# Kernel optimization log

Hardware: AMD Instinct MI355X
Metric: run time of the kernel (lower is better)

The kernel has to match this reference:

```python
import jax, jax.numpy as jnp
import numpy as np

B, S, D, H, E, K = 4, 2048, 1024, 512, 64, 8


def setup_inputs() -> dict:
    key = jax.random.key(0)
    k1, k2, k3, k4 = jax.random.split(key, 4)
    x = jax.random.normal(k1, (B, S, D), dtype=jnp.float32)
    # gate weight stored as [D, E] (equivalent to torch Linear weight [E, D] transposed)
    Wg = jax.random.normal(k2, (D, E), dtype=jnp.float32) * (1.0 / np.sqrt(D))
    Wup = jax.random.normal(k3, (E, D, H), dtype=jnp.float32) * (1.0 / np.sqrt(D))
    Wdown = jax.random.normal(k4, (E, H, D), dtype=jnp.float32) * (1.0 / np.sqrt(H))
    return {"x": x, "Wg": Wg, "Wup": Wup, "Wdown": Wdown}


def reference(x, Wg, Wup, Wdown):
    # NOTE: ExpertMLP.forward in the source ignores gate_proj: out = down(silu(up(x)))
    T = B * S
    flat = x.reshape(T, D)                        # [T, D]
    logits = flat @ Wg                            # [T, E]
    topk_scores, topk_idx = jax.lax.top_k(logits, K)   # [T, K]
    gate_w = jax.nn.softmax(topk_scores, axis=-1)       # [T, K]
    # dense combine matrix [T, E]; topk indices are unique per token
    rows = jnp.arange(T)[:, None]
    combine = jnp.zeros((T, E), dtype=x.dtype).at[rows, topk_idx].set(gate_w)
    # scan over experts: each expert runs on all tokens, masked/weighted by combine
    def body(acc, params):
        wu, wd, c = params                         # [D,H], [H,D], [T]
        h = jax.nn.silu(flat @ wu)                 # [T, H]
        y = h @ wd                                 # [T, D]
        return acc + c[:, None] * y, None
    out0 = jnp.zeros((T, D), dtype=x.dtype)
    out, _ = jax.lax.scan(body, out0, (Wup, Wdown, combine.T))
    return out.reshape(B, S, D)
```

## Files before the change

### kernel.cpp

```cpp
#include <hip/hip_runtime.h>
#include <hip/hip_bf16.h>
#include <stdint.h>
#include <math.h>

#define T_TOK 8192
#define DDIM  1024
#define HDIM  512
#define NEXP  64
#define TOPK  8
#define CHUNKS 16

typedef __bf16 bf16x8 __attribute__((ext_vector_type(8)));
typedef float  f32x4  __attribute__((ext_vector_type(4)));

__device__ __forceinline__ void load_lds16(const void* gp, void* lp){
  __builtin_amdgcn_global_load_lds(
      (__attribute__((address_space(1))) void*)(uintptr_t)gp,
      (__attribute__((address_space(3))) void*)lp, 16, 0, 0);
}

__device__ __forceinline__ unsigned short f2bfbits(float f){
  union { __bf16 b; unsigned short u; } cv; cv.b = (__bf16)f; return cv.u;
}
__device__ __forceinline__ float bf2f(unsigned short s){
  unsigned int u = ((unsigned int)s) << 16; return __uint_as_float(u);
}

__global__ __launch_bounds__(256) void k_cvt_x(const float* __restrict__ x,
                                               __bf16* __restrict__ xb){
  size_t i   = (size_t)blockIdx.x * 256 + threadIdx.x;
  size_t off = i * 8;
  float4 v0 = *(const float4*)(x + off);
  float4 v1 = *(const float4*)(x + off + 4);
  bf16x8 o;
  o[0]=(__bf16)v0.x; o[1]=(__bf16)v0.y; o[2]=(__bf16)v0.z; o[3]=(__bf16)v0.w;
  o[4]=(__bf16)v1.x; o[5]=(__bf16)v1.y; o[6]=(__bf16)v1.z; o[7]=(__bf16)v1.w;
  *(bf16x8*)(xb + off) = o;
}

__global__ __launch_bounds__(256) void k_transpose_cvt(const float* __restrict__ src,
                                                       __bf16* __restrict__ dst,
                                                       int R, int C){
  __shared__ float tile[32][33];
  int z  = blockIdx.z;
  int c0 = blockIdx.x * 32;
  int r0 = blockIdx.y * 32;
  const float* s = src + (size_t)z * R * C;
  __bf16*      d = dst + (size_t)z * R * C;
  int tx = threadIdx.x, ty = threadIdx.y;
  #pragma unroll
  for (int i = ty; i < 32; i += 8)
    tile[i][tx] = s[(size_t)(r0 + i) * C + c0 + tx];
  __syncthreads();
  #pragma unroll
  for (int i = ty; i < 32; i += 8)
    d[(size_t)(c0 + i) * R + r0 + tx] = (__bf16)tile[tx][i];
}

__global__ __launch_bounds__(256) void k_gate(const float* __restrict__ x,
                                              const float* __restrict__ Wg,
                                              float* __restrict__ logits){
  __shared__ float xs[32][64];
  __shared__ float ws[32][64];
  const int tid = threadIdx.x;
  const int m0  = blockIdx.x * 64;
  const int tm  = (tid >> 4) << 2;
  const int tn  = (tid & 15) << 2;
  const int sr  = tid >> 2;
  const int sc  = tid & 3;
  double acc[4][4];
  #pragma unroll
  for (int i=0;i<4;i++)
    #pragma unroll
    for (int j=0;j<4;j++) acc[i][j]=0.0;

  for (int k0 = 0; k0 < DDIM; k0 += 32){
    {
      const float4* g = (const float4*)(Wg + (size_t)k0 * 64);
      float4* l = (float4*)&ws[0][0];
      l[tid]       = g[tid];
      l[tid + 256] = g[tid + 256];
    }
    {
      const float* g = x + (size_t)(m0 + sr) * DDIM + k0 + sc * 8;
      float4 a = *(const float4*)g;
      float4 b = *(const float4*)(g + 4);
      xs[sc*8+0][sr]=a.x; xs[sc*8+1][sr]=a.y; xs[sc*8+2][sr]=a.z; xs[sc*8+3][sr]=a.w;
      xs[sc*8+4][sr]=b.x; xs[sc*8+5][sr]=b.y; xs[sc*8+6][sr]=b.z; xs[sc*8+7][sr]=b.w;
    }
    __syncthreads();
    for (int k = 0; k < 32; k++){
      float4 a4 = *(const float4*)&xs[k][tm];
      float4 b4 = *(const float4*)&ws[k][tn];
      float av[4] = {a4.x,a4.y,a4.z,a4.w};
      float bv[4] = {b4.x,b4.y,b4.z,b4.w};
      #pragma unroll
      for (int i=0;i<4;i++)
        #pragma unroll
        for (int j=0;j<4;j++)
          acc[i][j] += (double)av[i] * (double)bv[j];
    }
    __syncthreads();
  }
  #pragma unroll
  for (int i=0;i<4;i++){
    float4 o = make_float4((float)acc[i][0],(float)acc[i][1],(float)acc[i][2],(float)acc[i][3]);
    *(float4*)&logits[(size_t)(m0 + tm + i) * 64 + tn] = o;
  }
}

__global__ __launch_bounds__(256) void k_topk(const float* __restrict__ logits,
                                              int* __restrict__ tk_idx,
                                              float* __restrict__ tk_w){
  const int lane = threadIdx.x & 63;
  const int t    = blockIdx.x * 4 + (threadIdx.x >> 6);
  float v = logits[(size_t)t * 64 + lane];
  const int myi = lane;
  float mv[8]; int mi[8];
  #pragma unroll
  for (int k = 0; k < 8; k++){
    float bv = v; int bi = myi;
    #pragma unroll
    for (int off = 32; off > 0; off >>= 1){
      float ov = __shfl_xor(bv, off, 64);
      int   oi = __shfl_xor(bi, off, 64);
      if (ov > bv || (ov == bv && oi < bi)){ bv = ov; bi = oi; }
    }
    mv[k] = bv; mi[k] = bi;
    if (bi == myi) v = -INFINITY;
  }
  float w[8]; float s = 0.f;
  #pragma unroll
  for (int k = 0; k < 8; k++){ w[k] = expf(mv[k] - mv[0]); s += w[k]; }
  float inv = 1.0f / s;
  if (lane == 0){
    #pragma unroll
    for (int k = 0; k < 8; k++){
      tk_idx[(size_t)t * 8 + k] = mi[k];
      tk_w [(size_t)t * 8 + k] = w[k] * inv;
    }
  }
}

__global__ __launch_bounds__(256) void k_hist(const int* __restrict__ tk_idx,
                                              int* __restrict__ g_hist){
  __shared__ int h[4][64];
  const int tid = threadIdx.x, wave = tid >> 6;
  ((int*)h)[tid] = 0;
  __syncthreads();
  const int4* p = (const int4*)(tk_idx + blockIdx.x * 4096);
  #pragma unroll
  for (int i = 0; i < 4; i++){
    int4 v = p[i * 256 + tid];
    atomicAdd(&h[wave][v.x], 1); atomicAdd(&h[wave][v.y], 1);
    atomicAdd(&h[wave][v.z], 1); atomicAdd(&h[wave][v.w], 1);
  }
  __syncthreads();
  if (tid < 64)
    g_hist[blockIdx.x * 64 + tid] = h[0][tid] + h[1][tid] + h[2][tid] + h[3][tid];
}

__global__ void k_scan(const int* __restrict__ g_hist,
                       int* __restrict__ offsets,
                       int* __restrict__ g_base){
  const int e = threadIdx.x;
  int h[CHUNKS]; int tot = 0;
  #pragma unroll
  for (int c = 0; c < CHUNKS; c++){ h[c] = g_hist[c * 64 + e]; tot += h[c]; }
  int inc = tot;
  #pragma unroll
  for (int off = 1; off < 64; off <<= 1){
    int n = __shfl_up(inc, off, 64);
    if (e >= off) inc += n;
  }
  int exc = inc - tot;
  offsets[e] = exc;
  if (e == 63) offsets[64] = inc;
  int b = exc;
  #pragma unroll
  for (int c = 0; c < CHUNKS; c++){ g_base[c * 64 + e] = b; b += h[c]; }
}

__global__ __launch_bounds__(256) void k_scatter(const int* __restrict__ tk_idx,
                                                 const int* __restrict__ g_base,
                                                 int* __restrict__ slot_token,
                                                 int* __restrict__ inv_pos){
  __shared__ int cnt[64];
  const int tid = threadIdx.x;
  if (tid < 64) cnt[tid] = g_base[blockIdx.x * 64 + tid];
  __syncthreads();
  const int base = blockIdx.x * 4096;
  #pragma unroll
  for (int i = 0; i < 16; i++){
    int gid = base + i * 256 + tid;
    int e = tk_idx[gid];
    int pos = atomicAdd(&cnt[e], 1);
    slot_token[pos] = gid >> 3;
    inv_pos[gid] = pos;
  }
}


__global__ __launch_bounds__(512) void k_gemm1(const __bf16* __restrict__ xb,
                                               const __bf16* __restrict__ wupT,
                                               const int* __restrict__ offsets,
                                               const int* __restrict__ slot_token,
                                               __bf16* __restrict__ h){
  const int e    = blockIdx.z;
  const int base = offsets[e];
  const int ne   = offsets[e + 1] - base;
  const int m0   = blockIdx.x * 256;
  if (m0 >= ne) return;
  const int n0   = blockIdx.y * 256;

  __shared__ __align__(16) __bf16 As[2][256 * 64];
  __shared__ __align__(16) __bf16 Bs[2][256 * 64];
  __shared__ int s_tok[256];

  const int tid = threadIdx.x;
  if (tid < 256){
    int r = m0 + tid;
    s_tok[tid] = slot_token[base + (r < ne ? r : (ne - 1))];
  }
  __syncthreads();

  const int wave = tid >> 6, lane = tid & 63;
  const int wm = (wave >> 2) << 7;
  const int wn = (wave & 3) << 6;
  const int fr = lane & 15, kc = lane >> 4;
  const int rxor = fr & 7;
  const __bf16* wB = wupT + (size_t)e * HDIM * DDIM + (size_t)n0 * DDIM;

  const int srow = (wave << 3) + (lane >> 3);
  const int scol = (((lane & 7) ^ (lane >> 3)) << 3);
  const __bf16* gA[4]; const __bf16* gB[4]; int ldsOff[4];
  #pragma unroll
  for (int q = 0; q < 4; q++){
    int r = (q << 6) + srow;
    gA[q] = xb + (size_t)s_tok[r] * DDIM + scol;
    gB[q] = wB + (size_t)r * DDIM + scol;
    ldsOff[q] = (q << 12) + (wave << 9);
  }

  f32x4 acc[8][4];
  #pragma unroll
  for (int i=0;i<8;i++)
    #pragma unroll
    for (int j=0;j<4;j++) acc[i][j] = (f32x4){0.f,0.f,0.f,0.f};

  #pragma unroll
  for (int q = 0; q < 4; q++){
    load_lds16(gA[q], (void*)&As[0][ldsOff[q]]);
    load_lds16(gB[q], (void*)&Bs[0][ldsOff[q]]);
  }
  __syncthreads();

  const int NK = DDIM / 64;
  for (int t = 0; t < NK; ++t){
    const int cur = t & 1;
    if (t + 1 < NK){
      const int k1 = (t + 1) << 6;
      const int nxt = cur ^ 1;
      #pragma unroll
      for (int q = 0; q < 4; q++){
        load_lds16(gA[q] + k1, (void*)&As[nxt][ldsOff[q]]);
        load_lds16(gB[q] + k1, (void*)&Bs[nxt][ldsOff[q]]);
      }
    }
    #pragma unroll
    for (int ks = 0; ks < 2; ks++){
      const int cA = (((ks << 2) + kc) ^ rxor) << 3;
      bf16x8 af[8], bg[4];
      #pragma unroll
      for (int i=0;i<8;i++) af[i] = *(const bf16x8*)&As[cur][((wm + (i<<4) + fr) << 6) + cA];
      #pragma unroll
      for (int j=0;j<4;j++) bg[j] = *(const bf16x8*)&Bs[cur][((wn + (j<<4) + fr) << 6) + cA];
      #pragma unroll
      for (int i=0;i<8;i++)
        #pragma unroll
        for (int j=0;j<4;j++)
          acc[i][j] = __builtin_amdgcn_mfma_f32_16x16x32_bf16(af[i], bg[j], acc[i][j], 0, 0, 0);
    }
    __syncthreads();
  }

  const int cr = (lane >> 4) << 2, cc = lane & 15;
  #pragma unroll
  for (int i=0;i<8;i++){
    #pragma unroll
    for (int reg=0;reg<4;reg++){
      int rl = wm + (i << 4) + cr + reg;
      int gm = m0 + rl;
      if (gm < ne){
        __bf16* hrow = h + (size_t)(base + gm) * HDIM + n0 + wn;
        #pragma unroll
        for (int j=0;j<4;j++){
          float v  = acc[i][j][reg];
          float sv = v / (1.0f + __expf(-v));
          unsigned short u = f2bfbits(sv);
          int part = __shfl_xor((int)u, 1, 64);
          if (!(lane & 1)){
            unsigned int packed = ((unsigned int)(unsigned short)part << 16) | u;
            *(unsigned int*)((unsigned short*)hrow + (j << 4) + cc) = packed;
          }
        }
      }
    }
  }
}

__global__ __launch_bounds__(512) void k_gemm2(const __bf16* __restrict__ h,
                                               const __bf16* __restrict__ wdownT,
                                               const int* __restrict__ offsets,
                                               __bf16* __restrict__ y,
                                               int elo){
  const int e    = elo + blockIdx.z;
  const int base = offsets[e];
  const int ne   = offsets[e + 1] - base;
  const int m0   = blockIdx.x * 256;
  if (m0 >= ne) return;
  const int n0   = blockIdx.y * 256;
  const int ybase = offsets[elo];

  __shared__ __align__(16) __bf16 As[2][256 * 64];
  __shared__ __align__(16) __bf16 Bs[2][256 * 64];

  const int tid = threadIdx.x;
  const int wave = tid >> 6, lane = tid & 63;
  const int wm = (wave >> 2) << 7;
  const int wn = (wave & 3) << 6;
  const int fr = lane & 15, kc = lane >> 4;
  const int rxor = fr & 7;
  const __bf16* wB = wdownT + (size_t)e * DDIM * HDIM + (size_t)n0 * HDIM;

  const int srow = (wave << 3) + (lane >> 3);
  const int scol = (((lane & 7) ^ (lane >> 3)) << 3);
  const __bf16* gA[4]; const __bf16* gB[4]; int ldsOff[4];
  #pragma unroll
  for (int q = 0; q < 4; q++){
    int r = (q << 6) + srow;
    int sl = m0 + r; if (sl >= ne) sl = ne - 1;
    gA[q] = h + (size_t)(base + sl) * HDIM + scol;
    gB[q] = wB + (size_t)r * HDIM + scol;
    ldsOff[q] = (q << 12) + (wave << 9);
  }

  f32x4 acc[8][4];
  #pragma unroll
  for (int i=0;i<8;i++)
    #pragma unroll
    for (int j=0;j<4;j++) acc[i][j] = (f32x4){0.f,0.f,0.f,0.f};

  #pragma unroll
  for (int q = 0; q < 4; q++){
    load_lds16(gA[q], (void*)&As[0][ldsOff[q]]);
    load_lds16(gB[q], (void*)&Bs[0][ldsOff[q]]);
  }
  __syncthreads();

  const int NK = HDIM / 64;
  for (int t = 0; t < NK; ++t){
    const int cur = t & 1;
    if (t + 1 < NK){
      const int k1 = (t + 1) << 6;
      const int nxt = cur ^ 1;
      #pragma unroll
      for (int q = 0; q < 4; q++){
        load_lds16(gA[q] + k1, (void*)&As[nxt][ldsOff[q]]);
        load_lds16(gB[q] + k1, (void*)&Bs[nxt][ldsOff[q]]);
      }
    }
    #pragma unroll
    for (int ks = 0; ks < 2; ks++){
      const int cA = (((ks << 2) + kc) ^ rxor) << 3;
      bf16x8 af[8], bg[4];
      #pragma unroll
      for (int i=0;i<8;i++) af[i] = *(const bf16x8*)&As[cur][((wm + (i<<4) + fr) << 6) + cA];
      #pragma unroll
      for (int j=0;j<4;j++) bg[j] = *(const bf16x8*)&Bs[cur][((wn + (j<<4) + fr) << 6) + cA];
      #pragma unroll
      for (int i=0;i<8;i++)
        #pragma unroll
        for (int j=0;j<4;j++)
          acc[i][j] = __builtin_amdgcn_mfma_f32_16x16x32_bf16(af[i], bg[j], acc[i][j], 0, 0, 0);
    }
    __syncthreads();
  }

  const int cr = (lane >> 4) << 2, cc = lane & 15;
  #pragma unroll
  for (int i=0;i<8;i++){
    #pragma unroll
    for (int reg=0;reg<4;reg++){
      int rl = wm + (i << 4) + cr + reg;
      int gm = m0 + rl;
      if (gm < ne){
        __bf16* yrow = y + (size_t)(base - ybase + gm) * DDIM + n0 + wn;
        #pragma unroll
        for (int j=0;j<4;j++){
          unsigned short u = f2bfbits(acc[i][j][reg]);
          int part = __shfl_xor((int)u, 1, 64);
          if (!(lane & 1)){
            unsigned int packed = ((unsigned int)(unsigned short)part << 16) | u;
            *(unsigned int*)((unsigned short*)yrow + (j << 4) + cc) = packed;
          }
        }
      }
    }
  }
}

__global__ __launch_bounds__(256) void k_combine(const __bf16* __restrict__ y,
                                                 const int* __restrict__ tk_idx,
                                                 const float* __restrict__ tk_w,
                                                 const int* __restrict__ inv_pos,
                                                 const int* __restrict__ offsets,
                                                 float* __restrict__ out,
                                                 int elo, int ehi, int first){
  const int t   = blockIdx.x;
  const int tid = threadIdx.x;
  __shared__ int se[8]; __shared__ float sw[8]; __shared__ int sp[8];
  if (tid < 8){
    se[tid] = tk_idx[(size_t)t * 8 + tid];
    sw[tid] = tk_w [(size_t)t * 8 + tid];
    sp[tid] = inv_pos[(size_t)t * 8 + tid];
  }
  __syncthreads();
  const int ybase = offsets[elo];
  const int c = tid << 2;
  float4 acc;
  if (first) acc = make_float4(0.f, 0.f, 0.f, 0.f);
  else       acc = *(const float4*)&out[(size_t)t * DDIM + c];
  #pragma unroll
  for (int k = 0; k < 8; k++){
    int e = se[k];
    if (e >= elo && e < ehi){
      const unsigned short* yr = (const unsigned short*)y + (size_t)(sp[k] - ybase) * DDIM + c;
      ushort4 raw = *(const ushort4*)yr;
      float w = sw[k];
      acc.x += w * bf2f(raw.x);
      acc.y += w * bf2f(raw.y);
      acc.z += w * bf2f(raw.z);
      acc.w += w * bf2f(raw.w);
    }
  }
  *(float4*)&out[(size_t)t * DDIM + c] = acc;
}

extern "C" void kernel_launch(void* const* d_in, const int* in_sizes, int n_in,
                              void* d_out, int out_size, void* d_ws, size_t ws_size,
                              hipStream_t stream){
  const float* x     = (const float*)d_in[0];
  const float* Wg    = (const float*)d_in[1];
  const float* Wup   = (const float*)d_in[2];
  const float* Wdown = (const float*)d_in[3];
  float* out = (float*)d_out;

  char* ws = (char*)d_ws;
  size_t off = 0;
  auto alloc = [&](size_t bytes) -> void* {
    void* p = ws + off;
    off += (bytes + 255) & ~(size_t)255;
    return p;
  };
  __bf16* wupT      = (__bf16*)alloc((size_t)NEXP * DDIM * HDIM * 2);
  __bf16* xb        = (__bf16*)alloc((size_t)T_TOK * DDIM * 2);
  float*  logits    = (float*)alloc((size_t)T_TOK * NEXP * 4);
  __bf16* wdownT    = (__bf16*)alloc((size_t)NEXP * DDIM * HDIM * 2);
  __bf16* hbuf      = (__bf16*)alloc((size_t)T_TOK * TOPK * HDIM * 2);
  int*    tk_idx    = (int*)  alloc((size_t)T_TOK * TOPK * 4);
  float*  tk_w      = (float*)alloc((size_t)T_TOK * TOPK * 4);
  int*    slot_tok  = (int*)  alloc((size_t)T_TOK * TOPK * 4);
  int*    inv_pos   = (int*)  alloc((size_t)T_TOK * TOPK * 4);
  int*    g_hist    = (int*)  alloc((size_t)CHUNKS * 64 * 4);
  int*    g_base    = (int*)  alloc((size_t)CHUNKS * 64 * 4);
  int*    offsets   = (int*)  alloc(512);
  __bf16* ybuf      = (__bf16*)ws;

  k_cvt_x<<<4096, 256, 0, stream>>>(x, xb);
  k_transpose_cvt<<<dim3(16, 32, 64), dim3(32, 8), 0, stream>>>(Wup,   wupT,   DDIM, HDIM);
  k_transpose_cvt<<<dim3(32, 16, 64), dim3(32, 8), 0, stream>>>(Wdown, wdownT, HDIM, DDIM);
  k_gate<<<T_TOK / 64, 256, 0, stream>>>(x, Wg, logits);
  k_topk<<<T_TOK / 4, 256, 0, stream>>>(logits, tk_idx, tk_w);
  k_hist<<<CHUNKS, 256, 0, stream>>>(tk_idx, g_hist);
  k_scan<<<1, 64, 0, stream>>>(g_hist, offsets, g_base);
  k_scatter<<<CHUNKS, 256, 0, stream>>>(tk_idx, g_base, slot_tok, inv_pos);
  k_gemm1<<<dim3(8, 2, 64), 512, 0, stream>>>(xb, wupT, offsets, slot_tok, hbuf);
  k_gemm2<<<dim3(8, 4, 32), 512, 0, stream>>>(hbuf, wdownT, offsets, ybuf, 0);
  k_combine<<<T_TOK, 256, 0, stream>>>(ybuf, tk_idx, tk_w, inv_pos, offsets, out, 0, 32, 1);
  k_gemm2<<<dim3(8, 4, 32), 512, 0, stream>>>(hbuf, wdownT, offsets, ybuf, 32);
  k_combine<<<T_TOK, 256, 0, stream>>>(ybuf, tk_idx, tk_w, inv_pos, offsets, out, 32, 64, 0);
}
```

Baseline: 676.2 us.

## Split GEMM k-tiles into quadrant stages with fine-grained vmcnt waits

Both grouped GEMM kernels now load each k-tile in four half-tile stages: A and B rows are remapped so each staged half feeds one quadrant of the output. MFMA work on the current buffer is interleaved with these partial loads, using explicit s_waitcnt vmcnt counts, raw barriers, sched_barrier and setprio. The intent is to overlap global-to-LDS traffic with compute at a finer grain than whole-tile double buffering. This relies on the vmcnt counts exactly matching the outstanding loads per stage, and it adds more barriers per k-step.

```diff
diff --git a/kernel.cpp b/kernel.cpp
--- a/kernel.cpp
+++ b/kernel.cpp
@@ -25,6 +25,13 @@
 __device__ __forceinline__ float bf2f(unsigned short s){
   unsigned int u = ((unsigned int)s) << 16; return __uint_as_float(u);
 }
+
+#define VM6() asm volatile("s_waitcnt vmcnt(6)" ::: "memory")
+#define VM4() asm volatile("s_waitcnt vmcnt(4)" ::: "memory")
+#define VM2() asm volatile("s_waitcnt vmcnt(2)" ::: "memory")
+#define VM0() asm volatile("s_waitcnt vmcnt(0)" ::: "memory")
+#define BAR() __builtin_amdgcn_s_barrier()
+#define SB0() __builtin_amdgcn_sched_barrier(0)
 
 __global__ __launch_bounds__(256) void k_cvt_x(const float* __restrict__ x,
                                                __bf16* __restrict__ xb){
@@ -201,6 +208,32 @@
 }
 
 
+#define QUAD(MH, NH, buf, AS, BS) { \
+  bf16x8 qaf[4][2], qbg[2][2]; \
+  const int abase_ = ((MH) << 7) + (wm >> 1); \
+  const int bbase_ = ((NH) << 7) + (wn >> 1); \
+  _Pragma("unroll") for (int i = 0; i < 4; i++) \
+    _Pragma("unroll") for (int ks = 0; ks < 2; ks++) \
+      qaf[i][ks] = *(const bf16x8*)&AS[buf][((abase_ + (i<<4) + fr) << 6) + ((((ks<<2)+kc)^rxor)<<3)]; \
+  _Pragma("unroll") for (int j = 0; j < 2; j++) \
+    _Pragma("unroll") for (int ks = 0; ks < 2; ks++) \
+      qbg[j][ks] = *(const bf16x8*)&BS[buf][((bbase_ + (j<<4) + fr) << 6) + ((((ks<<2)+kc)^rxor)<<3)]; \
+  __builtin_amdgcn_s_setprio(1); \
+  _Pragma("unroll") for (int ks = 0; ks < 2; ks++) \
+    _Pragma("unroll") for (int i = 0; i < 4; i++) \
+      _Pragma("unroll") for (int j = 0; j < 2; j++) \
+        acc[((MH)<<2)+i][((NH)<<1)+j] = __builtin_amdgcn_mfma_f32_16x16x32_bf16( \
+            qaf[i][ks], qbg[j][ks], acc[((MH)<<2)+i][((NH)<<1)+j], 0, 0, 0); \
+  __builtin_amdgcn_s_setprio(0); \
+}
+
+__device__ __forceinline__ int lrA_map(int q, int srow){
+  return ((q & 1) << 7) + ((q >> 1) << 6) + srow;
+}
+__device__ __forceinline__ int lrB_map(int q, int srow){
+  return ((((q & 1) << 1) | (srow >> 5)) << 6) + ((q >> 1) << 5) + (srow & 31);
+}
+
 __global__ __launch_bounds__(512) void k_gemm1(const __bf16* __restrict__ xb,
                                                const __bf16* __restrict__ wupT,
                                                const int* __restrict__ offsets,
@@ -236,9 +269,8 @@
   const __bf16* gA[4]; const __bf16* gB[4]; int ldsOff[4];
   #pragma unroll
   for (int q = 0; q < 4; q++){
-    int r = (q << 6) + srow;
-    gA[q] = xb + (size_t)s_tok[r] * DDIM + scol;
-    gB[q] = wB + (size_t)r * DDIM + scol;
+    gA[q] = xb + (size_t)s_tok[lrA_map(q, srow)] * DDIM + scol;
+    gB[q] = wB + (size_t)lrB_map(q, srow) * DDIM + scol;
     ldsOff[q] = (q << 12) + (wave << 9);
   }
 
@@ -248,40 +280,32 @@
     #pragma unroll
     for (int j=0;j<4;j++) acc[i][j] = (f32x4){0.f,0.f,0.f,0.f};
 
-  #pragma unroll
-  for (int q = 0; q < 4; q++){
-    load_lds16(gA[q], (void*)&As[0][ldsOff[q]]);
-    load_lds16(gB[q], (void*)&Bs[0][ldsOff[q]]);
-  }
-  __syncthreads();
+  auto stA = [&](int buf, int hf, int koff){
+    load_lds16(gA[(hf<<1)]   + koff, (void*)&As[buf][ldsOff[(hf<<1)]]);
+    load_lds16(gA[(hf<<1)|1] + koff, (void*)&As[buf][ldsOff[(hf<<1)|1]]);
+  };
+  auto stB = [&](int buf, int hf, int koff){
+    load_lds16(gB[(hf<<1)]   + koff, (void*)&Bs[buf][ldsOff[(hf<<1)]]);
+    load_lds16(gB[(hf<<1)|1] + koff, (void*)&Bs[buf][ldsOff[(hf<<1)|1]]);
+  };
+
+  stA(0,0,0); stB(0,0,0); stA(0,1,0); stB(0,1,0);
 
   const int NK = DDIM / 64;
-  for (int t = 0; t < NK; ++t){
-    const int cur = t & 1;
-    if (t + 1 < NK){
-      const int k1 = (t + 1) << 6;
-      const int nxt = cur ^ 1;
-      #pragma unroll
-      for (int q = 0; q < 4; q++){
-        load_lds16(gA[q] + k1, (void*)&As[nxt][ldsOff[q]]);
-        load_lds16(gB[q] + k1, (void*)&Bs[nxt][ldsOff[q]]);
-      }
-    }
-    #pragma unroll
-    for (int ks = 0; ks < 2; ks++){
-      const int cA = (((ks << 2) + kc) ^ rxor) << 3;
-      bf16x8 af[8], bg[4];
-      #pragma unroll
-      for (int i=0;i<8;i++) af[i] = *(const bf16x8*)&As[cur][((wm + (i<<4) + fr) << 6) + cA];
-      #pragma unroll
-      for (int j=0;j<4;j++) bg[j] = *(const bf16x8*)&Bs[cur][((wn + (j<<4) + fr) << 6) + cA];
-      #pragma unroll
-      for (int i=0;i<8;i++)
-        #pragma unroll
-        for (int j=0;j<4;j++)
-          acc[i][j] = __builtin_amdgcn_mfma_f32_16x16x32_bf16(af[i], bg[j], acc[i][j], 0, 0, 0);
-    }
-    __syncthreads();
+  for (int t = 0; t < NK - 1; ++t){
+    const int p = t & 1, pn = p ^ 1;
+    const int k1 = (t + 1) << 6;
+    stA(pn,0,k1); VM6(); BAR(); SB0(); QUAD(0,0,p,As,Bs);
+    stB(pn,0,k1); VM6(); BAR(); SB0(); QUAD(1,0,p,As,Bs);
+    stA(pn,1,k1); VM6(); BAR(); SB0(); QUAD(0,1,p,As,Bs);
+    stB(pn,1,k1);        BAR(); SB0(); QUAD(1,1,p,As,Bs); BAR();
+  }
+  {
+    const int p = (NK - 1) & 1;
+    VM4(); BAR(); SB0(); QUAD(0,0,p,As,Bs);
+    VM2(); BAR(); SB0(); QUAD(1,0,p,As,Bs);
+    VM0(); BAR(); SB0(); QUAD(0,1,p,As,Bs);
+           BAR(); SB0(); QUAD(1,1,p,As,Bs);
   }
 
   const int cr = (lane >> 4) << 2, cc = lane & 15;
@@ -338,10 +362,10 @@
   const __bf16* gA[4]; const __bf16* gB[4]; int ldsOff[4];
   #pragma unroll
   for (int q = 0; q < 4; q++){
-    int r = (q << 6) + srow;
-    int sl = m0 + r; if (sl >= ne) sl = ne - 1;
+    int lr = lrA_map(q, srow);
+    int sl = m0 + lr; if (sl >= ne) sl = ne - 1;
     gA[q] = h + (size_t)(base + sl) * HDIM + scol;
-    gB[q] = wB + (size_t)r * HDIM + scol;
+    gB[q] = wB + (size_t)lrB_map(q, srow) * HDIM + scol;
     ldsOff[q] = (q << 12) + (wave << 9);
   }
 
@@ -351,40 +375,32 @@
     #pragma unroll
     for (int j=0;j<4;j++) acc[i][j] = (f32x4){0.f,0.f,0.f,0.f};
 
-  #pragma unroll
-  for (int q = 0; q < 4; q++){
-    load_lds16(gA[q], (void*)&As[0][ldsOff[q]]);
-    load_lds16(gB[q], (void*)&Bs[0][ldsOff[q]]);
-  }
-  __syncthreads();
+  auto stA = [&](int buf, int hf, int koff){
+    load_lds16(gA[(hf<<1)]   + koff, (void*)&As[buf][ldsOff[(hf<<1)]]);
+    load_lds16(gA[(hf<<1)|1] + koff, (void*)&As[buf][ldsOff[(hf<<1)|1]]);
+  };
+  auto stB = [&](int buf, int hf, int koff){
+    load_lds16(gB[(hf<<1)]   + koff, (void*)&Bs[buf][ldsOff[(hf<<1)]]);
+    load_lds16(gB[(hf<<1)|1] + koff, (void*)&Bs[buf][ldsOff[(hf<<1)|1]]);
+  };
+
+  stA(0,0,0); stB(0,0,0); stA(0,1,0); stB(0,1,0);
 
   const int NK = HDIM / 64;
-  for (int t = 0; t < NK; ++t){
-    const int cur = t & 1;
-    if (t + 1 < NK){
-      const int k1 = (t + 1) << 6;
-      const int nxt = cur ^ 1;
-      #pragma unroll
-      for (int q = 0; q < 4; q++){
-        load_lds16(gA[q] + k1, (void*)&As[nxt][ldsOff[q]]);
-        load_lds16(gB[q] + k1, (void*)&Bs[nxt][ldsOff[q]]);
-      }
-    }
-    #pragma unroll
-    for (int ks = 0; ks < 2; ks++){
-      const int cA = (((ks << 2) + kc) ^ rxor) << 3;
-      bf16x8 af[8], bg[4];
-      #pragma unroll
-      for (int i=0;i<8;i++) af[i] = *(const bf16x8*)&As[cur][((wm + (i<<4) + fr) << 6) + cA];
-      #pragma unroll
-      for (int j=0;j<4;j++) bg[j] = *(const bf16x8*)&Bs[cur][((wn + (j<<4) + fr) << 6) + cA];
-      #pragma unroll
-      for (int i=0;i<8;i++)
-        #pragma unroll
-        for (int j=0;j<4;j++)
-          acc[i][j] = __builtin_amdgcn_mfma_f32_16x16x32_bf16(af[i], bg[j], acc[i][j], 0, 0, 0);
-    }
-    __syncthreads();
+  for (int t = 0; t < NK - 1; ++t){
+    const int p = t & 1, pn = p ^ 1;
+    const int k1 = (t + 1) << 6;
+    stA(pn,0,k1); VM6(); BAR(); SB0(); QUAD(0,0,p,As,Bs);
+    stB(pn,0,k1); VM6(); BAR(); SB0(); QUAD(1,0,p,As,Bs);
+    stA(pn,1,k1); VM6(); BAR(); SB0(); QUAD(0,1,p,As,Bs);
+    stB(pn,1,k1);        BAR(); SB0(); QUAD(1,1,p,As,Bs); BAR();
+  }
+  {
+    const int p = (NK - 1) & 1;
+    VM4(); BAR(); SB0(); QUAD(0,0,p,As,Bs);
+    VM2(); BAR(); SB0(); QUAD(1,0,p,As,Bs);
+    VM0(); BAR(); SB0(); QUAD(0,1,p,As,Bs);
+           BAR(); SB0(); QUAD(1,1,p,As,Bs);
   }
 
   const int cr = (lane >> 4) << 2, cc = lane & 15;
```

After: 703.1 us. 4.0% more time.

## Use persistent 1D grid with XCD-aware block remap for grouped expert GEMMs

Applied to the files above, without the earlier changes.

Replaces the 3D grid (m-tile, n-tile, expert) with a fixed 512-block 1D grid. Block ids are remapped so consecutive ids spread across the 8 XCDs, and each block loops over m-tiles in strides of 1024 rows. This removes the many early-exit empty blocks when expert token counts are uneven, and it keeps the tiles of one expert together on an XCD to improve L2 reuse of expert weights. In exchange, experts with many tokens are handled serially by fewer blocks, which can cause load imbalance. The order of the two weight transpose launches is also swapped.

```diff
diff --git a/kernel.cpp b/kernel.cpp
--- a/kernel.cpp
+++ b/kernel.cpp
@@ -206,24 +206,20 @@
                                                const int* __restrict__ offsets,
                                                const int* __restrict__ slot_token,
                                                __bf16* __restrict__ h){
-  const int e    = blockIdx.z;
+  const int bid = blockIdx.x;
+  const int L   = ((bid & 7) << 6) | (bid >> 3);
+  const int mb  = L & 3;
+  const int nb  = (L >> 2) & 1;
+  const int e   = L >> 3;
   const int base = offsets[e];
   const int ne   = offsets[e + 1] - base;
-  const int m0   = blockIdx.x * 256;
-  if (m0 >= ne) return;
-  const int n0   = blockIdx.y * 256;
+  const int n0   = nb << 8;
 
   __shared__ __align__(16) __bf16 As[2][256 * 64];
   __shared__ __align__(16) __bf16 Bs[2][256 * 64];
   __shared__ int s_tok[256];
 
   const int tid = threadIdx.x;
-  if (tid < 256){
-    int r = m0 + tid;
-    s_tok[tid] = slot_token[base + (r < ne ? r : (ne - 1))];
-  }
-  __syncthreads();
-
   const int wave = tid >> 6, lane = tid & 63;
   const int wm = (wave >> 2) << 7;
   const int wn = (wave & 3) << 6;
@@ -233,75 +229,88 @@
 
   const int srow = (wave << 3) + (lane >> 3);
   const int scol = (((lane & 7) ^ (lane >> 3)) << 3);
-  const __bf16* gA[4]; const __bf16* gB[4]; int ldsOff[4];
+  const __bf16* gB[4]; int ldsOff[4];
   #pragma unroll
   for (int q = 0; q < 4; q++){
-    int r = (q << 6) + srow;
-    gA[q] = xb + (size_t)s_tok[r] * DDIM + scol;
-    gB[q] = wB + (size_t)r * DDIM + scol;
+    gB[q] = wB + (size_t)((q << 6) + srow) * DDIM + scol;
     ldsOff[q] = (q << 12) + (wave << 9);
   }
 
-  f32x4 acc[8][4];
-  #pragma unroll
-  for (int i=0;i<8;i++)
-    #pragma unroll
-    for (int j=0;j<4;j++) acc[i][j] = (f32x4){0.f,0.f,0.f,0.f};
-
-  #pragma unroll
-  for (int q = 0; q < 4; q++){
-    load_lds16(gA[q], (void*)&As[0][ldsOff[q]]);
-    load_lds16(gB[q], (void*)&Bs[0][ldsOff[q]]);
-  }
-  __syncthreads();
-
-  const int NK = DDIM / 64;
-  for (int t = 0; t < NK; ++t){
-    const int cur = t & 1;
-    if (t + 1 < NK){
-      const int k1 = (t + 1) << 6;
-      const int nxt = cur ^ 1;
-      #pragma unroll
-      for (int q = 0; q < 4; q++){
-        load_lds16(gA[q] + k1, (void*)&As[nxt][ldsOff[q]]);
-        load_lds16(gB[q] + k1, (void*)&Bs[nxt][ldsOff[q]]);
+  const int cr = (lane >> 4) << 2, cc = lane & 15;
+
+  for (int m0 = mb << 8; m0 < ne; m0 += 1024){
+    __syncthreads();
+    if (tid < 256){
+      int r = m0 + tid;
+      s_tok[tid] = slot_token[base + (r < ne ? r : (ne - 1))];
+    }
+    __syncthreads();
+
+    const __bf16* gA[4];
+    #pragma unroll
+    for (int q = 0; q < 4; q++)
+      gA[q] = xb + (size_t)s_tok[(q << 6) + srow] * DDIM + scol;
+
+    f32x4 acc[8][4];
+    #pragma unroll
+    for (int i=0;i<8;i++)
+      #pragma unroll
+      for (int j=0;j<4;j++) acc[i][j] = (f32x4){0.f,0.f,0.f,0.f};
+
+    #pragma unroll
+    for (int q = 0; q < 4; q++){
+      load_lds16(gA[q], (void*)&As[0][ldsOff[q]]);
+      load_lds16(gB[q], (void*)&Bs[0][ldsOff[q]]);
+    }
+    __syncthreads();
+
+    const int NK = DDIM / 64;
+    for (int t = 0; t < NK; ++t){
+      const int cur = t & 1;
+      if (t + 1 < NK){
+        const int k1 = (t + 1) << 6;
+        const int nxt = cur ^ 1;
+        #pragma unroll
+        for (int q = 0; q < 4; q++){
+          load_lds16(gA[q] + k1, (void*)&As[nxt][ldsOff[q]]);
+          load_lds16(gB[q] + k1, (void*)&Bs[nxt][ldsOff[q]]);
+        }
       }
-    }
-    #pragma unroll
-    for (int ks = 0; ks < 2; ks++){
-      const int cA = (((ks << 2) + kc) ^ rxor) << 3;
-      bf16x8 af[8], bg[4];
-      #pragma unroll
-      for (int i=0;i<8;i++) af[i] = *(const bf16x8*)&As[cur][((wm + (i<<4) + fr) << 6) + cA];
-      #pragma unroll
-      for (int j=0;j<4;j++) bg[j] = *(const bf16x8*)&Bs[cur][((wn + (j<<4) + fr) << 6) + cA];
-      #pragma unroll
-      for (int i=0;i<8;i++)
-        #pragma unroll
-        for (int j=0;j<4;j++)
-          acc[i][j] = __builtin_amdgcn_mfma_f32_16x16x32_bf16(af[i], bg[j], acc[i][j], 0, 0, 0);
-    }
-    __syncthreads();
-  }
-
-  const int cr = (lane >> 4) << 2, cc = lane & 15;
-  #pragma unroll
-  for (int i=0;i<8;i++){
-    #pragma unroll
-    for (int reg=0;reg<4;reg++){
-      int rl = wm + (i << 4) + cr + reg;
-      int gm = m0 + rl;
-      if (gm < ne){
-        __bf16* hrow = h + (size_t)(base + gm) * HDIM + n0 + wn;
-        #pragma unroll
-        for (int j=0;j<4;j++){
-          float v  = acc[i][j][reg];
-          float sv = v / (1.0f + __expf(-v));
-          unsigned short u = f2bfbits(sv);
-          int part = __shfl_xor((int)u, 1, 64);
-          if (!(lane & 1)){
-            unsigned int packed = ((unsigned int)(unsigned short)part << 16) | u;
-            *(unsigned int*)((unsigned short*)hrow + (j << 4) + cc) = packed;
+      #pragma unroll
+      for (int ks = 0; ks < 2; ks++){
+        const int cA = (((ks << 2) + kc) ^ rxor) << 3;
+        bf16x8 af[8], bg[4];
+        #pragma unroll
+        for (int i=0;i<8;i++) af[i] = *(const bf16x8*)&As[cur][((wm + (i<<4) + fr) << 6) + cA];
+        #pragma unroll
+        for (int j=0;j<4;j++) bg[j] = *(const bf16x8*)&Bs[cur][((wn + (j<<4) + fr) << 6) + cA];
+        #pragma unroll
+        for (int i=0;i<8;i++)
+          #pragma unroll
+          for (int j=0;j<4;j++)
+            acc[i][j] = __builtin_amdgcn_mfma_f32_16x16x32_bf16(af[i], bg[j], acc[i][j], 0, 0, 0);
+      }
+      __syncthreads();
+    }
+
+    #pragma unroll
+    for (int i=0;i<8;i++){
+      #pragma unroll
+      for (int reg=0;reg<4;reg++){
+        int rl = wm + (i << 4) + cr + reg;
+        int gm = m0 + rl;
+        if (gm < ne){
+          __bf16* hrow = h + (size_t)(base + gm) * HDIM + n0 + wn;
+          #pragma unroll
+          for (int j=0;j<4;j++){
+            float v  = acc[i][j][reg];
+            float sv = v / (1.0f + __expf(-v));
+            unsigned short u = f2bfbits(sv);
+            int part = __shfl_xor((int)u, 1, 64);
+            if (!(lane & 1)){
+              unsigned int packed = ((unsigned int)(unsigned short)part << 16) | u;
+              *(unsigned int*)((unsigned short*)hrow + (j << 4) + cc) = packed;
+            }
           }
         }
       }
@@ -314,12 +323,14 @@
                                                const int* __restrict__ offsets,
                                                __bf16* __restrict__ y,
                                                int elo){
-  const int e    = elo + blockIdx.z;
+  const int bid = blockIdx.x;
+  const int L   = ((bid & 7) << 6) | (bid >> 3);
+  const int mb  = L & 3;
+  const int nb  = (L >> 2) & 3;
+  const int e   = elo + (L >> 4);
   const int base = offsets[e];
   const int ne   = offsets[e + 1] - base;
-  const int m0   = blockIdx.x * 256;
-  if (m0 >= ne) return;
-  const int n0   = blockIdx.y * 256;
+  const int n0   = nb << 8;
   const int ybase = offsets[elo];
 
   __shared__ __align__(16) __bf16 As[2][256 * 64];
@@ -335,74 +346,82 @@
 
   const int srow = (wave << 3) + (lane >> 3);
   const int scol = (((lane & 7) ^ (lane >> 3)) << 3);
-  const __bf16* gA[4]; const __bf16* gB[4]; int ldsOff[4];
+  const __bf16* gB[4]; int ldsOff[4];
   #pragma unroll
   for (int q = 0; q < 4; q++){
-    int r = (q << 6) + srow;
-    int sl = m0 + r; if (sl >= ne) sl = ne - 1;
-    gA[q] = h + (size_t)(base + sl) * HDIM + scol;
-    gB[q] = wB + (size_t)r * HDIM + scol;
+    gB[q] = wB + (size_t)((q << 6) + srow) * HDIM + scol;
     ldsOff[q] = (q << 12) + (wave << 9);
   }
 
-  f32x4 acc[8][4];
-  #pragma unroll
-  for (int i=0;i<8;i++)
-    #pragma unroll
-    for (int j=0;j<4;j++) acc[i][j] = (f32x4){0.f,0.f,0.f,0.f};
-
-  #pragma unroll
-  for (int q = 0; q < 4; q++){
-    load_lds16(gA[q], (void*)&As[0][ldsOff[q]]);
-    load_lds16(gB[q], (void*)&Bs[0][ldsOff[q]]);
-  }
-  __syncthreads();
-
-  const int NK = HDIM / 64;
-  for (int t = 0; t < NK; ++t){
-    const int cur = t & 1;
-    if (t + 1 < NK){
-      const int k1 = (t + 1) << 6;
-      const int nxt = cur ^ 1;
-      #pragma unroll
-      for (int q = 0; q < 4; q++){
-        load_lds16(gA[q] + k1, (void*)&As[nxt][ldsOff[q]]);
-        load_lds16(gB[q] + k1, (void*)&Bs[nxt][ldsOff[q]]);
+  const int cr = (lane >> 4) << 2, cc = lane & 15;
+
+  for (int m0 = mb << 8; m0 < ne; m0 += 1024){
+    const __bf16* gA[4];
+    #pragma unroll
+    for (int q = 0; q < 4; q++){
+      int sl = m0 + (q << 6) + srow; if (sl >= ne) sl = ne - 1;
+      gA[q] = h + (size_t)(base + sl) * HDIM + scol;
+    }
+
+    f32x4 acc[8][4];
+    #pragma unroll
+    for (int i=0;i<8;i++)
+      #pragma unroll
+      for (int j=0;j<4;j++) acc[i][j] = (f32x4){0.f,0.f,0.f,0.f};
+
+    __syncthreads();
+    #pragma unroll
+    for (int q = 0; q < 4; q++){
+      load_lds16(gA[q], (void*)&As[0][ldsOff[q]]);
+      load_lds16(gB[q], (void*)&Bs[0][ldsOff[q]]);
+    }
+    __syncthreads();
+
+    const int NK = HDIM / 64;
+    for (int t = 0; t < NK; ++t){
+      const int cur = t & 1;
+      if (t + 1 < NK){
+        const int k1 = (t + 1) << 6;
+        const int nxt = cur ^ 1;
+        #pragma unroll
+        for (int q = 0; q < 4; q++){
+          load_lds16(gA[q] + k1, (void*)&As[nxt][ldsOff[q]]);
+          load_lds16(gB[q] + k1, (void*)&Bs[nxt][ldsOff[q]]);
+        }
       }
-    }
-    #pragma unroll
-    for (int ks = 0; ks < 2; ks++){
-      const int cA = (((ks << 2) + kc) ^ rxor) << 3;
-      bf16x8 af[8], bg[4];
-      #pragma unroll
-      for (int i=0;i<8;i++) af[i] = *(const bf16x8*)&As[cur][((wm + (i<<4) + fr) << 6) + cA];
-      #pragma unroll
-      for (int j=0;j<4;j++) bg[j] = *(const bf16x8*)&Bs[cur][((wn + (j<<4) + fr) << 6) + cA];
-      #pragma unroll
-      for (int i=0;i<8;i++)
-        #pragma unroll
-        for (int j=0;j<4;j++)
-          acc[i][j] = __builtin_amdgcn_mfma_f32_16x16x32_bf16(af[i], bg[j], acc[i][j], 0, 0, 0);
-    }
-    __syncthreads();
-  }
-
-  const int cr = (lane >> 4) << 2, cc = lane & 15;
-  #pragma unroll
-  for (int i=0;i<8;i++){
-    #pragma unroll
-    for (int reg=0;reg<4;reg++){
-      int rl = wm + (i << 4) + cr + reg;
-      int gm = m0 + rl;
-      if (gm < ne){
-        __bf16* yrow = y + (size_t)(base - ybase + gm) * DDIM + n0 + wn;
-        #pragma unroll
-        for (int j=0;j<4;j++){
-          unsigned short u = f2bfbits(acc[i][j][reg]);
-          int part = __shfl_xor((int)u, 1, 64);
-          if (!(lane & 1)){
-            unsigned int packed = ((unsigned int)(unsigned short)part << 16) | u;
-            *(unsigned int*)((unsigned short*)yrow + (j << 4) + cc) = packed;
+      #pragma unroll
+      for (int ks = 0; ks < 2; ks++){
+        const int cA = (((ks << 2) + kc) ^ rxor) << 3;
+        bf16x8 af[8], bg[4];
+        #pragma unroll
+        for (int i=0;i<8;i++) af[i] = *(const bf16x8*)&As[cur][((wm + (i<<4) + fr) << 6) + cA];
+        #pragma unroll
+        for (int j=0;j<4;j++) bg[j] = *(const bf16x8*)&Bs[cur][((wn + (j<<4) + fr) << 6) + cA];
+        #pragma unroll
+        for (int i=0;i<8;i++)
+          #pragma unroll
+          for (int j=0;j<4;j++)
+            acc[i][j] = __builtin_amdgcn_mfma_f32_16x16x32_bf16(af[i], bg[j], acc[i][j], 0, 0, 0);
+      }
+      __syncthreads();
+    }
+
+    #pragma unroll
+    for (int i=0;i<8;i++){
+      #pragma unroll
+      for (int reg=0;reg<4;reg++){
+        int rl = wm + (i << 4) + cr + reg;
+        int gm = m0 + rl;
+        if (gm < ne){
+          __bf16* yrow = y + (size_t)(base - ybase + gm) * DDIM + n0 + wn;
+          #pragma unroll
+          for (int j=0;j<4;j++){
+            unsigned short u = f2bfbits(acc[i][j][reg]);
+            int part = __shfl_xor((int)u, 1, 64);
+            if (!(lane & 1)){
+              unsigned int packed = ((unsigned int)(unsigned short)part << 16) | u;
+              *(unsigned int*)((unsigned short*)yrow + (j << 4) + cc) = packed;
+            }
           }
         }
       }
@@ -478,16 +497,16 @@
   __bf16* ybuf      = (__bf16*)ws;
 
   k_cvt_x<<<4096, 256, 0, stream>>>(x, xb);
+  k_transpose_cvt<<<dim3(32, 16, 64), dim3(32, 8), 0, stream>>>(Wdown, wdownT, HDIM, DDIM);
   k_transpose_cvt<<<dim3(16, 32, 64), dim3(32, 8), 0, stream>>>(Wup,   wupT,   DDIM, HDIM);
-  k_transpose_cvt<<<dim3(32, 16, 64), dim3(32, 8), 0, stream>>>(Wdown, wdownT, HDIM, DDIM);
   k_gate<<<T_TOK / 64, 256, 0, stream>>>(x, Wg, logits);
   k_topk<<<T_TOK / 4, 256, 0, stream>>>(logits, tk_idx, tk_w);
   k_hist<<<CHUNKS, 256, 0, stream>>>(tk_idx, g_hist);
   k_scan<<<1, 64, 0, stream>>>(g_hist, offsets, g_base);
   k_scatter<<<CHUNKS, 256, 0, stream>>>(tk_idx, g_base, slot_tok, inv_pos);
-  k_gemm1<<<dim3(8, 2, 64), 512, 0, stream>>>(xb, wupT, offsets, slot_tok, hbuf);
-  k_gemm2<<<dim3(8, 4, 32), 512, 0, stream>>>(hbuf, wdownT, offsets, ybuf, 0);
+  k_gemm1<<<512, 512, 0, stream>>>(xb, wupT, offsets, slot_tok, hbuf);
+  k_gemm2<<<512, 512, 0, stream>>>(hbuf, wdownT, offsets, ybuf, 0);
   k_combine<<<T_TOK, 256, 0, stream>>>(ybuf, tk_idx, tk_w, inv_pos, offsets, out, 0, 32, 1);
-  k_gemm2<<<dim3(8, 4, 32), 512, 0, stream>>>(hbuf, wdownT, offsets, ybuf, 32);
+  k_gemm2<<<512, 512, 0, stream>>>(hbuf, wdownT, offsets, ybuf, 32);
   k_combine<<<T_TOK, 256, 0, stream>>>(ybuf, tk_idx, tk_w, inv_pos, offsets, out, 32, 64, 0);
 }
```

After: 667.6 us. No clear change (-1.3%).

## Shrink grouped GEMM tiles to 128x128x32 with 1D swizzled persistent-style grid

Applied to the files above, without the earlier changes.

Both expert GEMMs move from 256x256 tiles with BK=64 and 512 threads to 128x128 tiles with BK=32 and 256 threads, with launch bounds allowing four blocks per CU. A flattened 1D grid with an XCD-aware block remap assigns each block an expert, an N tile and an M stripe, and the block loops over M tiles in steps of 1024 rows. Early-exit empty blocks are replaced by blocks that stride through rows. This targets better occupancy and load balance across uneven expert sizes, but gives up the per-tile data reuse of the larger tiles. The LDS swizzle is adapted to the new 32-wide rows, and the order of the two weight transposes is swapped.

```diff
diff --git a/kernel.cpp b/kernel.cpp
--- a/kernel.cpp
+++ b/kernel.cpp
@@ -201,107 +201,115 @@
 }
 
 
-__global__ __launch_bounds__(512) void k_gemm1(const __bf16* __restrict__ xb,
-                                               const __bf16* __restrict__ wupT,
-                                               const int* __restrict__ offsets,
-                                               const int* __restrict__ slot_token,
-                                               __bf16* __restrict__ h){
-  const int e    = blockIdx.z;
+__global__ __launch_bounds__(256, 4) void k_gemm1(const __bf16* __restrict__ xb,
+                                                  const __bf16* __restrict__ wupT,
+                                                  const int* __restrict__ offsets,
+                                                  const int* __restrict__ slot_token,
+                                                  __bf16* __restrict__ h){
+  const int bid = blockIdx.x;
+  const int L   = ((bid & 7) << 8) | (bid >> 3);
+  const int e   = L >> 5;
+  const int mb  = L & 7;
+  const int nb  = (L >> 3) & 3;
   const int base = offsets[e];
   const int ne   = offsets[e + 1] - base;
-  const int m0   = blockIdx.x * 256;
-  if (m0 >= ne) return;
-  const int n0   = blockIdx.y * 256;
-
-  __shared__ __align__(16) __bf16 As[2][256 * 64];
-  __shared__ __align__(16) __bf16 Bs[2][256 * 64];
-  __shared__ int s_tok[256];
+  const int n0   = nb << 7;
+
+  __shared__ __align__(16) __bf16 As[2][128 * 32];
+  __shared__ __align__(16) __bf16 Bs[2][128 * 32];
+  __shared__ int s_tok[128];
 
   const int tid = threadIdx.x;
-  if (tid < 256){
-    int r = m0 + tid;
-    s_tok[tid] = slot_token[base + (r < ne ? r : (ne - 1))];
-  }
-  __syncthreads();
-
   const int wave = tid >> 6, lane = tid & 63;
-  const int wm = (wave >> 2) << 7;
-  const int wn = (wave & 3) << 6;
+  const int wm = (wave >> 1) << 6;
+  const int wn = (wave & 1) << 6;
   const int fr = lane & 15, kc = lane >> 4;
-  const int rxor = fr & 7;
+  const int rxor = (fr & 3) ^ ((fr >> 2) & 3);
   const __bf16* wB = wupT + (size_t)e * HDIM * DDIM + (size_t)n0 * DDIM;
 
-  const int srow = (wave << 3) + (lane >> 3);
-  const int scol = (((lane & 7) ^ (lane >> 3)) << 3);
-  const __bf16* gA[4]; const __bf16* gB[4]; int ldsOff[4];
-  #pragma unroll
-  for (int q = 0; q < 4; q++){
-    int r = (q << 6) + srow;
-    gA[q] = xb + (size_t)s_tok[r] * DDIM + scol;
+  const int srl  = lane >> 2;
+  const int sxor = (srl & 3) ^ ((srl >> 2) & 3);
+  const int scol = ((lane & 3) ^ sxor) << 3;
+  const __bf16* gB[2]; int ldsOff[2];
+  #pragma unroll
+  for (int q = 0; q < 2; q++){
+    int r = (q << 6) + (wave << 4) + srl;
     gB[q] = wB + (size_t)r * DDIM + scol;
-    ldsOff[q] = (q << 12) + (wave << 9);
-  }
-
-  f32x4 acc[8][4];
-  #pragma unroll
-  for (int i=0;i<8;i++)
-    #pragma unroll
-    for (int j=0;j<4;j++) acc[i][j] = (f32x4){0.f,0.f,0.f,0.f};
-
-  #pragma unroll
-  for (int q = 0; q < 4; q++){
-    load_lds16(gA[q], (void*)&As[0][ldsOff[q]]);
-    load_lds16(gB[q], (void*)&Bs[0][ldsOff[q]]);
-  }
-  __syncthreads();
-
-  const int NK = DDIM / 64;
-  for (int t = 0; t < NK; ++t){
-    const int cur = t & 1;
-    if (t + 1 < NK){
-      const int k1 = (t + 1) << 6;
-      const int nxt = cur ^ 1;
-      #pragma unroll
-      for (int q = 0; q < 4; q++){
-        load_lds16(gA[q] + k1, (void*)&As[nxt][ldsOff[q]]);
-        load_lds16(gB[q] + k1, (void*)&Bs[nxt][ldsOff[q]]);
+    ldsOff[q] = (q << 11) + (wave << 9);
+  }
+
+  const int cr = (lane >> 4) << 2, cc = lane & 15;
+
+  for (int m0 = mb << 7; m0 < ne; m0 += 1024){
+    __syncthreads();
+    if (tid < 128){
+      int r = m0 + tid;
+      s_tok[tid] = slot_token[base + (r < ne ? r : (ne - 1))];
+    }
+    __syncthreads();
+
+    const __bf16* gA[2];
+    #pragma unroll
+    for (int q = 0; q < 2; q++)
+      gA[q] = xb + (size_t)s_tok[(q << 6) + (wave << 4) + srl] * DDIM + scol;
+
+    f32x4 acc[4][4];
+    #pragma unroll
+    for (int i=0;i<4;i++)
+      #pragma unroll
+      for (int j=0;j<4;j++) acc[i][j] = (f32x4){0.f,0.f,0.f,0.f};
+
+    #pragma unroll
+    for (int q = 0; q < 2; q++){
+      load_lds16(gA[q], (void*)&As[0][ldsOff[q]]);
+      load_lds16(gB[q], (void*)&Bs[0][ldsOff[q]]);
+    }
+    __syncthreads();
+
+    const int NK = DDIM / 32;
+    for (int t = 0; t < NK; ++t){
+      const int cur = t & 1;
+      if (t + 1 < NK){
+        const int k1 = (t + 1) << 5;
+        const int nxt = cur ^ 1;
+        #pragma unroll
+        for (int q = 0; q < 2; q++){
+          load_lds16(gA[q] + k1, (void*)&As[nxt][ldsOff[q]]);
+          load_lds16(gB[q] + k1, (void*)&Bs[nxt][ldsOff[q]]);
+        }
       }
-    }
-    #pragma unroll
-    for (int ks = 0; ks < 2; ks++){
-      const int cA = (((ks << 2) + kc) ^ rxor) << 3;
-      bf16x8 af[8], bg[4];
-      #pragma unroll
-      for (int i=0;i<8;i++) af[i] = *(const bf16x8*)&As[cur][((wm + (i<<4) + fr) << 6) + cA];
-      #pragma unroll
-      for (int j=0;j<4;j++) bg[j] = *(const bf16x8*)&Bs[cur][((wn + (j<<4) + fr) << 6) + cA];
-      #pragma unroll
-      for (int i=0;i<8;i++)
+      const int cA = (kc ^ rxor) << 3;
+      bf16x8 af[4], bg[4];
+      #pragma unroll
+      for (int i=0;i<4;i++) af[i] = *(const bf16x8*)&As[cur][((wm + (i<<4) + fr) << 5) + cA];
+      #pragma unroll
+      for (int j=0;j<4;j++) bg[j] = *(const bf16x8*)&Bs[cur][((wn + (j<<4) + fr) << 5) + cA];
+      #pragma unroll
+      for (int i=0;i<4;i++)
         #pragma unroll
         for (int j=0;j<4;j++)
           acc[i][j] = __builtin_amdgcn_mfma_f32_16x16x32_bf16(af[i], bg[j], acc[i][j], 0, 0, 0);
-    }
-    __syncthreads();
-  }
-
-  const int cr = (lane >> 4) << 2, cc = lane & 15;
-  #pragma unroll
-  for (int i=0;i<8;i++){
-    #pragma unroll
-    for (int reg=0;reg<4;reg++){
-      int rl = wm + (i << 4) + cr + reg;
-      int gm = m0 + rl;
-      if (gm < ne){
-        __bf16* hrow = h + (size_t)(base + gm) * HDIM + n0 + wn;
-        #pragma unroll
-        for (int j=0;j<4;j++){
-          float v  = acc[i][j][reg];
-          float sv = v / (1.0f + __expf(-v));
-          unsigned short u = f2bfbits(sv);
-          int part = __shfl_xor((int)u, 1, 64);
-          if (!(lane & 1)){
-            unsigned int packed = ((unsigned int)(unsigned short)part << 16) | u;
-            *(unsigned int*)((unsigned short*)hrow + (j << 4) + cc) = packed;
+      __syncthreads();
+    }
+
+    #pragma unroll
+    for (int i=0;i<4;i++){
+      #pragma unroll
+      for (int reg=0;reg<4;reg++){
+        int rl = wm + (i << 4) + cr + reg;
+        int gm = m0 + rl;
+        if (gm < ne){
+          __bf16* hrow = h + (size_t)(base + gm) * HDIM + n0 + wn;
+          #pragma unroll
+          for (int j=0;j<4;j++){
+            float v  = acc[i][j][reg];
+            float sv = v / (1.0f + __expf(-v));
+            unsigned short u = f2bfbits(sv);
+            int part = __shfl_xor((int)u, 1, 64);
+            if (!(lane & 1)){
+              unsigned int packed = ((unsigned int)(unsigned short)part << 16) | u;
+              *(unsigned int*)((unsigned short*)hrow + (j << 4) + cc) = packed;
+            }
           }
         }
       }
@@ -309,100 +317,109 @@
   }
 }
 
-__global__ __launch_bounds__(512) void k_gemm2(const __bf16* __restrict__ h,
-                                               const __bf16* __restrict__ wdownT,
-                                               const int* __restrict__ offsets,
-                                               __bf16* __restrict__ y,
-                                               int elo){
-  const int e    = elo + blockIdx.z;
+__global__ __launch_bounds__(256, 4) void k_gemm2(const __bf16* __restrict__ h,
+                                                  const __bf16* __restrict__ wdownT,
+                                                  const int* __restrict__ offsets,
+                                                  __bf16* __restrict__ y,
+                                                  int elo){
+  const int bid = blockIdx.x;
+  const int L   = ((bid & 7) << 8) | (bid >> 3);
+  const int e   = elo + (L >> 6);
+  const int mb  = L & 7;
+  const int nb  = (L >> 3) & 7;
   const int base = offsets[e];
   const int ne   = offsets[e + 1] - base;
-  const int m0   = blockIdx.x * 256;
-  if (m0 >= ne) return;
-  const int n0   = blockIdx.y * 256;
+  const int n0   = nb << 7;
   const int ybase = offsets[elo];
 
-  __shared__ __align__(16) __bf16 As[2][256 * 64];
-  __shared__ __align__(16) __bf16 Bs[2][256 * 64];
+  __shared__ __align__(16) __bf16 As[2][128 * 32];
+  __shared__ __align__(16) __bf16 Bs[2][128 * 32];
 
   const int tid = threadIdx.x;
   const int wave = tid >> 6, lane = tid & 63;
-  const int wm = (wave >> 2) << 7;
-  const int wn = (wave & 3) << 6;
+  const int wm = (wave >> 1) << 6;
+  const int wn = (wave & 1) << 6;
   const int fr = lane & 15, kc = lane >> 4;
-  const int rxor = fr & 7;
+  const int rxor = (fr & 3) ^ ((fr >> 2) & 3);
   const __bf16* wB = wdownT + (size_t)e * DDIM * HDIM + (size_t)n0 * HDIM;
 
-  const int srow = (wave << 3) + (lane >> 3);
-  const int scol = (((lane & 7) ^ (lane >> 3)) << 3);
-  const __bf16* gA[4]; const __bf16* gB[4]; int ldsOff[4];
-  #pragma unroll
-  for (int q = 0; q < 4; q++){
-    int r = (q << 6) + srow;
-    int sl = m0 + r; if (sl >= ne) sl = ne - 1;
-    gA[q] = h + (size_t)(base + sl) * HDIM + scol;
+  const int srl  = lane >> 2;
+  const int sxor = (srl & 3) ^ ((srl >> 2) & 3);
+  const int scol = ((lane & 3) ^ sxor) << 3;
+  const __bf16* gB[2]; int ldsOff[2];
+  #pragma unroll
+  for (int q = 0; q < 2; q++){
+    int r = (q << 6) + (wave << 4) + srl;
     gB[q] = wB + (size_t)r * HDIM + scol;
-    ldsOff[q] = (q << 12) + (wave << 9);
-  }
-
-  f32x4 acc[8][4];
-  #pragma unroll
-  for (int i=0;i<8;i++)
-    #pragma unroll
-    for (int j=0;j<4;j++) acc[i][j] = (f32x4){0.f,0.f,0.f,0.f};
-
-  #pragma unroll
-  for (int q = 0; q < 4; q++){
-    load_lds16(gA[q], (void*)&As[0][ldsOff[q]]);
-    load_lds16(gB[q], (void*)&Bs[0][ldsOff[q]]);
-  }
-  __syncthreads();
-
-  const int NK = HDIM / 64;
-  for (int t = 0; t < NK; ++t){
-    const int cur = t & 1;
-    if (t + 1 < NK){
-      const int k1 = (t + 1) << 6;
-      const int nxt = cur ^ 1;
-      #pragma unroll
-      for (int q = 0; q < 4; q++){
-        load_lds16(gA[q] + k1, (void*)&As[nxt][ldsOff[q]]);
-        load_lds16(gB[q] + k1, (void*)&Bs[nxt][ldsOff[q]]);
+    ldsOff[q] = (q << 11) + (wave << 9);
+  }
+
+  const int cr = (lane >> 4) << 2, cc = lane & 15;
+
+  for (int m0 = mb << 7; m0 < ne; m0 += 1024){
+    const __bf16* gA[2];
+    #pragma unroll
+    for (int q = 0; q < 2; q++){
+      int sl = m0 + (q << 6) + (wave << 4) + srl; if (sl >= ne) sl = ne - 1;
+      gA[q] = h + (size_t)(base + sl) * HDIM + scol;
+    }
+
+    f32x4 acc[4][4];
+    #pragma unroll
+    for (int i=0;i<4;i++)
+      #pragma unroll
+      for (int j=0;j<4;j++) acc[i][j] = (f32x4){0.f,0.f,0.f,0.f};
+
+    __syncthreads();
+    #pragma unroll
+    for (int q = 0; q < 2; q++){
+      load_lds16(gA[q], (void*)&As[0][ldsOff[q]]);
+      load_lds16(gB[q], (void*)&Bs[0][ldsOff[q]]);
+    }
+    __syncthreads();
+
+    const int NK = HDIM / 32;
+    for (int t = 0; t < NK; ++t){
+      const int cur = t & 1;
+      if (t + 1 < NK){
+        const int k1 = (t + 1) << 5;
+        const int nxt = cur ^ 1;
+        #pragma unroll
+        for (int q = 0; q < 2; q++){
+          load_lds16(gA[q] + k1, (void*)&As[nxt][ldsOff[q]]);
+          load_lds16(gB[q] + k1, (void*)&Bs[nxt][ldsOff[q]]);
+        }
       }
-    }
-    #pragma unroll
-    for (int ks = 0; ks < 2; ks++){
-      const int cA = (((ks << 2) + kc) ^ rxor) << 3;
-      bf16x8 af[8], bg[4];
-      #pragma unroll
-      for (int i=0;i<8;i++) af[i] = *(const bf16x8*)&As[cur][((wm + (i<<4) + fr) << 6) + cA];
-      #pragma unroll
-      for (int j=0;j<4;j++) bg[j] = *(const bf16x8*)&Bs[cur][((wn + (j<<4) + fr) << 6) + cA];
-      #pragma unroll
-      for (int i=0;i<8;i++)
+      const int cA = (kc ^ rxor) << 3;
+      bf16x8 af[4], bg[4];
+      #pragma unroll
+      for (int i=0;i<4;i++) af[i] = *(const bf16x8*)&As[cur][((wm + (i<<4) + fr) << 5) + cA];
+      #pragma unroll
+      for (int j=0;j<4;j++) bg[j] = *(const bf16x8*)&Bs[cur][((wn + (j<<4) + fr) << 5) + cA];
+      #pragma unroll
+      for (int i=0;i<4;i++)
         #pragma unroll
         for (int j=0;j<4;j++)
           acc[i][j] = __builtin_amdgcn_mfma_f32_16x16x32_bf16(af[i], bg[j], acc[i][j], 0, 0, 0);
-    }
-    __syncthreads();
-  }
-
-  const int cr = (lane >> 4) << 2, cc = lane & 15;
-  #pragma unroll
-  for (int i=0;i<8;i++){
-    #pragma unroll
-    for (int reg=0;reg<4;reg++){
-      int rl = wm + (i << 4) + cr + reg;
-      int gm = m0 + rl;
-      if (gm < ne){
-        __bf16* yrow = y + (size_t)(base - ybase + gm) * DDIM + n0 + wn;
-        #pragma unroll
-        for (int j=0;j<4;j++){
-          unsigned short u = f2bfbits(acc[i][j][reg]);
-          int part = __shfl_xor((int)u, 1, 64);
-          if (!(lane & 1)){
-            unsigned int packed = ((unsigned int)(unsigned short)part << 16) | u;
-            *(unsigned int*)((unsigned short*)yrow + (j << 4) + cc) = packed;
+      __syncthreads();
+    }
+
+    #pragma unroll
+    for (int i=0;i<4;i++){
+      #pragma unroll
+      for (int reg=0;reg<4;reg++){
+        int rl = wm + (i << 4) + cr + reg;
+        int gm = m0 + rl;
+        if (gm < ne){
+          __bf16* yrow = y + (size_t)(base - ybase + gm) * DDIM + n0 + wn;
+          #pragma unroll
+          for (int j=0;j<4;j++){
+            unsigned short u = f2bfbits(acc[i][j][reg]);
+            int part = __shfl_xor((int)u, 1, 64);
+            if (!(lane & 1)){
+              unsigned int packed = ((unsigned int)(unsigned short)part << 16) | u;
+              *(unsigned int*)((unsigned short*)yrow + (j << 4) + cc) = packed;
+            }
           }
         }
       }
@@ -478,16 +495,16 @@
   __bf16* ybuf      = (__bf16*)ws;
 
   k_cvt_x<<<4096, 256, 0, stream>>>(x, xb);
+  k_transpose_cvt<<<dim3(32, 16, 64), dim3(32, 8), 0, stream>>>(Wdown, wdownT, HDIM, DDIM);
   k_transpose_cvt<<<dim3(16, 32, 64), dim3(32, 8), 0, stream>>>(Wup,   wupT,   DDIM, HDIM);
-  k_transpose_cvt<<<dim3(32, 16, 64), dim3(32, 8), 0, stream>>>(Wdown, wdownT, HDIM, DDIM);
   k_gate<<<T_TOK / 64, 256, 0, stream>>>(x, Wg, logits);
   k_topk<<<T_TOK / 4, 256, 0, stream>>>(logits, tk_idx, tk_w);
   k_hist<<<CHUNKS, 256, 0, stream>>>(tk_idx, g_hist);
   k_scan<<<1, 64, 0, stream>>>(g_hist, offsets, g_base);
   k_scatter<<<CHUNKS, 256, 0, stream>>>(tk_idx, g_base, slot_tok, inv_pos);
-  k_gemm1<<<dim3(8, 2, 64), 512, 0, stream>>>(xb, wupT, offsets, slot_tok, hbuf);
-  k_gemm2<<<dim3(8, 4, 32), 512, 0, stream>>>(hbuf, wdownT, offsets, ybuf, 0);
+  k_gemm1<<<2048, 256, 0, stream>>>(xb, wupT, offsets, slot_tok, hbuf);
+  k_gemm2<<<2048, 256, 0, stream>>>(hbuf, wdownT, offsets, ybuf, 0);
   k_combine<<<T_TOK, 256, 0, stream>>>(ybuf, tk_idx, tk_w, inv_pos, offsets, out, 0, 32, 1);
-  k_gemm2<<<dim3(8, 4, 32), 512, 0, stream>>>(hbuf, wdownT, offsets, ybuf, 32);
+  k_gemm2<<<2048, 256, 0, stream>>>(hbuf, wdownT, offsets, ybuf, 32);
   k_combine<<<T_TOK, 256, 0, stream>>>(ybuf, tk_idx, tk_w, inv_pos, offsets, out, 32, 64, 0);
 }
```

New measurement: 711.4 us. 1.05x slower.
